# Performance work log

Hardware: AMD Instinct MI355X
Metric: run time of the kernel (lower is better)

Reference implementation:

```python
import jax, jax.numpy as jnp
import numpy as np

N = 50000      # nodes
E = 800000     # edges
NIN = 512      # input features
NHID = 128     # hidden
NCLS = 64      # classes


def setup_inputs() -> dict:
    key = jax.random.key(0)
    k0, k1, k2, k3 = jax.random.split(key, 4)
    x = jax.random.normal(k0, (N, NIN), dtype=jnp.float32)
    edge_index = jax.random.randint(k1, (2, E), 0, N, dtype=jnp.int64)
    # Glorot-style init for GCNConv linear weights (bias starts at zero in PyG)
    W1 = jax.random.normal(k2, (NIN, NHID), dtype=jnp.float32) * (1.0 / np.sqrt(NIN))
    W2 = jax.random.normal(k3, (NHID, NCLS), dtype=jnp.float32) * (1.0 / np.sqrt(NHID))
    b1 = jnp.zeros((NHID,), dtype=jnp.float32)
    b2 = jnp.zeros((NCLS,), dtype=jnp.float32)
    return {"x": x, "edge_index": edge_index, "W1": W1, "b1": b1, "W2": W2, "b2": b2}


def gcn_conv(x, W, b, src, dst, n):
    """PyG GCNConv: linear transform, then sym-normalized aggregation with self-loops."""
    xw = x @ W                                                  # [n, out]
    ones = jnp.ones(src.shape[0], dtype=xw.dtype)
    deg = jax.ops.segment_sum(ones, dst, num_segments=n) + 1.0  # +1 for self-loop
    dinv = jax.lax.rsqrt(deg)                                   # deg >= 1
    norm = dinv[src] * dinv[dst]                                # [E]
    agg = jax.ops.segment_sum(xw[src] * norm[:, None], dst, num_segments=n)
    agg = agg + (dinv * dinv)[:, None] * xw                     # self-loop messages
    return agg + b


def reference(x, edge_index, W1, b1, W2, b2):
    src, dst = edge_index[0], edge_index[1]
    n = x.shape[0]
    # eval mode: dropout is a no-op; bn is defined but unused in forward
    h = gcn_conv(x, W1, b1, src, dst, n)
    h = jax.nn.relu(h)
    o = gcn_conv(h, W2, b2, src, dst, n)
    return jax.nn.log_softmax(o, axis=1)
```

## Files before the change

### kernel.cpp

```cpp
#include <hip/hip_runtime.h>
#include <hip/hip_bf16.h>
#include <cstdint>
#include <cstddef>

#define NNODES 50000
#define NEDGES 800000
#define NIN    512
#define NHID   128
#define NCLS   64

#define SCAN_BLK 512
#define SCAN_NB ((NNODES + SCAN_BLK - 1) / SCAN_BLK)

typedef __attribute__((ext_vector_type(8))) short bf16x8;
typedef __attribute__((ext_vector_type(4))) float f32x4;

static __device__ __forceinline__ ushort f2bf(float f) {
    uint32_t u = __float_as_uint(f);
    uint32_t r = (u + 0x7fffu + ((u >> 16) & 1u)) >> 16;
    return (ushort)r;
}
static __device__ __forceinline__ float bf2f(ushort b) {
    return __uint_as_float(((uint32_t)b) << 16);
}

__global__ void clear_kernel(int4* __restrict__ p, int n4) {
    int i = blockIdx.x * blockDim.x + threadIdx.x;
    if (i < n4) p[i] = make_int4(0, 0, 0, 0);
}


__global__ void deg_kernel(const int* __restrict__ dst, int* __restrict__ deg) {
    int e = blockIdx.x * blockDim.x + threadIdx.x;
    if (e < NEDGES) atomicAdd(&deg[dst[e]], 1);
}

__global__ __launch_bounds__(SCAN_BLK) void scan1_kernel(const int* __restrict__ deg,
                                                         int* __restrict__ blkSum,
                                                         float* __restrict__ dinv) {
    int i = blockIdx.x * SCAN_BLK + threadIdx.x;
    int d = (i < NNODES) ? deg[i] : 0;
    if (i < NNODES) dinv[i] = rsqrtf((float)d + 1.0f);
    int v = d;
#pragma unroll
    for (int off = 32; off; off >>= 1) v += __shfl_xor(v, off, 64);
    __shared__ int ws[SCAN_BLK / 64];
    int w = threadIdx.x >> 6;
    if ((threadIdx.x & 63) == 0) ws[w] = v;
    __syncthreads();
    if (threadIdx.x == 0) {
        int s = 0;
#pragma unroll
        for (int k = 0; k < SCAN_BLK / 64; ++k) s += ws[k];
        blkSum[blockIdx.x] = s;
    }
}

__global__ void scan2_kernel(int* __restrict__ blkSum, int* __restrict__ rowptr) {
    __shared__ int sh[128];
    int t = threadIdx.x;
    int v = (t < SCAN_NB) ? blkSum[t] : 0;
    sh[t] = v;
    __syncthreads();
    for (int off = 1; off < 128; off <<= 1) {
        int o = (t >= off) ? sh[t - off] : 0;
        __syncthreads();
        sh[t] += o;
        __syncthreads();
    }
    if (t < SCAN_NB) blkSum[t] = sh[t] - v;
    if (t == 0) rowptr[NNODES] = NEDGES;
}

__global__ __launch_bounds__(SCAN_BLK) void scan3_kernel(const int* __restrict__ deg,
                                                         const int* __restrict__ blkOff,
                                                         int* __restrict__ rowptr) {
    int i = blockIdx.x * SCAN_BLK + threadIdx.x;
    int v = (i < NNODES) ? deg[i] : 0;
    int lane = threadIdx.x & 63;
    int w = threadIdx.x >> 6;
    int inc = v;
#pragma unroll
    for (int off = 1; off < 64; off <<= 1) {
        int o = __shfl_up(inc, off, 64);
        if (lane >= off) inc += o;
    }
    __shared__ int ws[SCAN_BLK / 64];
    if (lane == 63) ws[w] = inc;
    __syncthreads();
    int wpre = 0;
    for (int k = 0; k < w; ++k) wpre += ws[k];
    if (i < NNODES) rowptr[i] = inc - v + wpre + blkOff[blockIdx.x];
}

__global__ void scatter_kernel(const int* __restrict__ src, const int* __restrict__ dst,
                               const int* __restrict__ rowptr, int* __restrict__ cursor,
                               const float* __restrict__ dinv, int2* __restrict__ csr) {
    int e = blockIdx.x * blockDim.x + threadIdx.x;
    if (e >= NEDGES) return;
    int d = dst[e];
    int s = src[e];
    int pos = rowptr[d] + atomicAdd(&cursor[d], 1);
    csr[pos] = make_int2(s, __float_as_int(dinv[s]));
}

template <int NOUT, int KS, int CF>
__global__ void pack_kernel(const float* __restrict__ W, ushort* __restrict__ pack) {
    int t = blockIdx.x * blockDim.x + threadIdx.x;
    if (t >= KS * CF * 64 * 8) return;
    int j = t & 7;
    int lane = (t >> 3) & 63;
    int cf = (t >> 9) % CF;
    int ks = t / (CF * 512);
    int k = ks * 32 + (lane >> 4) * 8 + j;
    int c = cf * 16 + (lane & 15);
    pack[t] = f2bf(W[(size_t)k * NOUT + c]);
}

__global__ __launch_bounds__(256) void gemm1_kernel(const float* __restrict__ A,
                                                    const ushort* __restrict__ packB,
                                                    ushort* __restrict__ C) {
    __shared__ float lds[2][64 * 64];
    const int t = threadIdx.x;
    const int lane = t & 63;
    const int w = t >> 6;
    const int rowBase = blockIdx.x * 64;
    const int rl = lane & 15;
    const int kg = lane >> 4;

    const int Rloc = (w << 2) + (lane >> 4);
    const int csw = ((lane & 15) << 4) ^ ((Rloc & 7) << 4);
    const char* Abase = (const char*)A;

    const int xr = (rl & 7) << 4;

    f32x4 acc[8];
#pragma unroll
    for (int cf = 0; cf < 8; ++cf) acc[cf] = (f32x4)(0.f);

    auto stage = [&](int buf, int chunk) {
#pragma unroll
        for (int r = 0; r < 4; ++r) {
            int row = rowBase + r * 16 + Rloc;
            if (row > NNODES - 1) row = NNODES - 1;
            const char* src = Abase + (size_t)row * (NIN * 4) + chunk * 256 + csw;
            char* dst = (char*)&lds[buf][0] + r * 4096 + w * 1024 + lane * 16;
            __builtin_amdgcn_global_load_lds((const uint32_t*)src, (uint32_t*)dst, 16, 0, 0);
        }
    };

    stage(0, 0);
    int buf = 0;
#pragma unroll
    for (int tch = 0; tch < 8; ++tch) {
        __syncthreads();
        if (tch + 1 < 8) stage(buf ^ 1, tch + 1);
        const char* lrow = (const char*)&lds[buf][0] + (w * 16 + rl) * 256;
#pragma unroll
        for (int ks = 0; ks < 2; ++ks) {
            float4 x0 = *(const float4*)(lrow + ((ks * 128 + kg * 32) ^ xr));
            float4 x1 = *(const float4*)(lrow + ((ks * 128 + kg * 32 + 16) ^ xr));
            bf16x8 af;
            af[0] = (short)f2bf(x0.x); af[1] = (short)f2bf(x0.y);
            af[2] = (short)f2bf(x0.z); af[3] = (short)f2bf(x0.w);
            af[4] = (short)f2bf(x1.x); af[5] = (short)f2bf(x1.y);
            af[6] = (short)f2bf(x1.z); af[7] = (short)f2bf(x1.w);
            const ushort* bpp = packB + ((size_t)(tch * 2 + ks) * 8) * 512 + (size_t)lane * 8;
#pragma unroll
            for (int cf = 0; cf < 8; ++cf) {
                bf16x8 bfv = *(const bf16x8*)(bpp + cf * 512);
                acc[cf] = __builtin_amdgcn_mfma_f32_16x16x32_bf16(af, bfv, acc[cf], 0, 0, 0);
            }
        }
        buf ^= 1;
    }
    const int rowW = rowBase + w * 16;
#pragma unroll
    for (int cf = 0; cf < 8; ++cf)
#pragma unroll
        for (int j = 0; j < 4; ++j) {
            int rr = rowW + kg * 4 + j;
            if (rr < NNODES) C[(size_t)rr * NHID + cf * 16 + rl] = f2bf(acc[cf][j]);
        }
}

__global__ __launch_bounds__(256) void gemm2_kernel(const ushort* __restrict__ A,
                                                    const ushort* __restrict__ packB,
                                                    ushort* __restrict__ C) {
    int wid = (blockIdx.x * blockDim.x + threadIdx.x) >> 6;
    int lane = threadIdx.x & 63;
    int rowBase = wid * 16;
    if (rowBase >= NNODES) return;
    int rl = lane & 15;
    int kg = lane >> 4;
    const ushort* ap = A + (size_t)(rowBase + rl) * NHID + kg * 8;

    f32x4 acc[4];
#pragma unroll
    for (int cf = 0; cf < 4; ++cf) acc[cf] = (f32x4)(0.f);

#pragma unroll
    for (int ks = 0; ks < 4; ++ks) {
        bf16x8 af = *(const bf16x8*)(ap + ks * 32);
        const ushort* bp = packB + ((size_t)(ks * 4) * 64 + lane) * 8;
#pragma unroll
        for (int cf = 0; cf < 4; ++cf) {
            bf16x8 bf = *(const bf16x8*)(bp + (size_t)cf * 512);
            acc[cf] = __builtin_amdgcn_mfma_f32_16x16x32_bf16(af, bf, acc[cf], 0, 0, 0);
        }
    }
#pragma unroll
    for (int cf = 0; cf < 4; ++cf)
#pragma unroll
        for (int j = 0; j < 4; ++j)
            C[(size_t)(rowBase + kg * 4 + j) * NCLS + cf * 16 + rl] = f2bf(acc[cf][j]);
}

__global__ __launch_bounds__(256) void agg1_kernel(const ushort* __restrict__ xw,
                                                   const int* __restrict__ rowptr,
                                                   const int2* __restrict__ csr,
                                                   const float* __restrict__ dinv,
                                                   const float* __restrict__ b1,
                                                   ushort* __restrict__ h) {
    int wid = (blockIdx.x * blockDim.x + threadIdx.x) >> 6;
    int lane = threadIdx.x & 63;
    if (wid >= NNODES) return;
    int beg = rowptr[wid], end = rowptr[wid + 1];
    float a0 = 0.f, a1 = 0.f;
    int j = beg;
    for (; j + 8 <= end; j += 8) {
        int2 e[8];
#pragma unroll
        for (int q = 0; q < 8; ++q) e[q] = csr[j + q];
        uint v[8];
#pragma unroll
        for (int q = 0; q < 8; ++q) v[q] = *(const uint*)&xw[(size_t)e[q].x * NHID + lane * 2];
#pragma unroll
        for (int q = 0; q < 8; ++q) {
            float wq = __int_as_float(e[q].y);
            a0 += wq * __uint_as_float(v[q] << 16);
            a1 += wq * __uint_as_float(v[q] & 0xffff0000u);
        }
    }
    for (; j < end; ++j) {
        int2 e = csr[j];
        float w = __int_as_float(e.y);
        uint v = *(const uint*)&xw[(size_t)e.x * NHID + lane * 2];
        a0 += w * __uint_as_float(v << 16);
        a1 += w * __uint_as_float(v & 0xffff0000u);
    }
    float di = dinv[wid];
    float sl = di * di;
    uint xv = *(const uint*)&xw[(size_t)wid * NHID + lane * 2];
    float2 bv = *(const float2*)&b1[lane * 2];
    float r0 = di * a0 + sl * __uint_as_float(xv << 16) + bv.x;
    float r1 = di * a1 + sl * __uint_as_float(xv & 0xffff0000u) + bv.y;
    uint o = (uint)f2bf(fmaxf(r0, 0.f)) | ((uint)f2bf(fmaxf(r1, 0.f)) << 16);
    *(uint*)&h[(size_t)wid * NHID + lane * 2] = o;
}

__global__ __launch_bounds__(256) void agg2_kernel(const ushort* __restrict__ xw,
                                                   const int* __restrict__ rowptr,
                                                   const int2* __restrict__ csr,
                                                   const float* __restrict__ dinv,
                                                   const float* __restrict__ b2,
                                                   float* __restrict__ out) {
    int wid = (blockIdx.x * blockDim.x + threadIdx.x) >> 6;
    int lane = threadIdx.x & 63;
    if (wid >= NNODES) return;
    int beg = rowptr[wid], end = rowptr[wid + 1];
    float a = 0.f;
    int j = beg;
    for (; j + 8 <= end; j += 8) {
        int2 e[8];
#pragma unroll
        for (int q = 0; q < 8; ++q) e[q] = csr[j + q];
        float v[8];
#pragma unroll
        for (int q = 0; q < 8; ++q) v[q] = bf2f(xw[(size_t)e[q].x * NCLS + lane]);
#pragma unroll
        for (int q = 0; q < 8; ++q) a += __int_as_float(e[q].y) * v[q];
    }
    for (; j < end; ++j) {
        int2 e = csr[j];
        a += __int_as_float(e.y) * bf2f(xw[(size_t)e.x * NCLS + lane]);
    }
    float di = dinv[wid];
    float o = di * a + di * di * bf2f(xw[(size_t)wid * NCLS + lane]) + b2[lane];
    float m = o;
#pragma unroll
    for (int off = 32; off; off >>= 1) m = fmaxf(m, __shfl_xor(m, off, 64));
    float ex = __expf(o - m);
    float ssum = ex;
#pragma unroll
    for (int off = 32; off; off >>= 1) ssum += __shfl_xor(ssum, off, 64);
    out[(size_t)wid * NCLS + lane] = (o - m) - __logf(ssum);
}


extern "C" void kernel_launch(void* const* d_in, const int* in_sizes, int n_in,
                              void* d_out, int out_size, void* d_ws, size_t ws_size,
                              hipStream_t stream) {
    const float* x  = (const float*)d_in[0];
    const int*   ei = (const int*)d_in[1];
    const int*   src = ei;
    const int*   dst = ei + NEDGES;
    const float* W1 = (const float*)d_in[2];
    const float* b1 = (const float*)d_in[3];
    const float* W2 = (const float*)d_in[4];
    const float* b2 = (const float*)d_in[5];
    float* out = (float*)d_out;

    char* w = (char*)d_ws;
    auto alloc = [&](size_t bytes) {
        char* p = w;
        w += (bytes + 255) & ~(size_t)255;
        return p;
    };
    int*    deg    = (int*)alloc((size_t)2 * NNODES * 4);
    int*    cursor = deg + NNODES;
    int*    rowptr = (int*)alloc((NNODES + 1) * 4);
    int*    blkSum = (int*)alloc(SCAN_NB * 4);
    int2*   csr    = (int2*)alloc((size_t)NEDGES * 8);
    float*  dinv   = (float*)alloc(NNODES * 4);
    ushort* pack1  = (ushort*)alloc((size_t)16 * 8 * 64 * 8 * 2);
    ushort* pack2  = (ushort*)alloc((size_t)4 * 4 * 64 * 8 * 2);
    ushort* xw1    = (ushort*)alloc((size_t)NNODES * NHID * 2);
    ushort* h      = (ushort*)alloc((size_t)NNODES * NHID * 2);
    ushort* xw2    = (ushort*)alloc((size_t)NNODES * NCLS * 2);

    const int n4 = (2 * NNODES + 3) / 4;
    clear_kernel<<<(n4 + 255) / 256, 256, 0, stream>>>((int4*)deg, n4);

    deg_kernel<<<(NEDGES + 255) / 256, 256, 0, stream>>>(dst, deg);
    scan1_kernel<<<SCAN_NB, SCAN_BLK, 0, stream>>>(deg, blkSum, dinv);
    scan2_kernel<<<1, 128, 0, stream>>>(blkSum, rowptr);
    scan3_kernel<<<SCAN_NB, SCAN_BLK, 0, stream>>>(deg, blkSum, rowptr);
    scatter_kernel<<<(NEDGES + 255) / 256, 256, 0, stream>>>(src, dst, rowptr, cursor, dinv, csr);

    pack_kernel<NHID, 16, 8><<<(16 * 8 * 64 * 8 + 255) / 256, 256, 0, stream>>>(W1, pack1);
    pack_kernel<NCLS, 4, 4><<<(4 * 4 * 64 * 8 + 255) / 256, 256, 0, stream>>>(W2, pack2);

    gemm1_kernel<<<(NNODES + 63) / 64, 256, 0, stream>>>(x, pack1, xw1);
    agg1_kernel<<<(NNODES * 64 + 255) / 256, 256, 0, stream>>>(xw1, rowptr, csr, dinv, b1, h);

    gemm2_kernel<<<(NNODES / 16 + 3) / 4, 256, 0, stream>>>(h, pack2, xw2);
    agg2_kernel<<<(NNODES * 64 + 255) / 256, 256, 0, stream>>>(xw2, rowptr, csr, dinv, b2, out);
}
```

Before: 209.5 us.

## Split gemm1 K across waves with LDS reduction instead of LDS-staged row tiles

Restructures the first GEMM so each block handles 16 rows, with each of the 4 waves taking a 128-wide K slice. Each wave loads its x values directly from global memory into registers, and the partial MFMA accumulators are reduced through shared memory by wave 0. This removes the double-buffered global_load_lds staging and its per-chunk barriers, and puts all of x's loads in flight at once. The cost is more blocks, B fragments re-read by every block (four times less reuse per block), a reduction step, and wave 0 alone writing the output.

```diff
diff --git a/kernel.cpp b/kernel.cpp
--- a/kernel.cpp
+++ b/kernel.cpp
@@ -120,68 +120,62 @@
 __global__ __launch_bounds__(256) void gemm1_kernel(const float* __restrict__ A,
                                                     const ushort* __restrict__ packB,
                                                     ushort* __restrict__ C) {
-    __shared__ float lds[2][64 * 64];
+    __shared__ f32x4 red[3][8][64];
     const int t = threadIdx.x;
     const int lane = t & 63;
     const int w = t >> 6;
-    const int rowBase = blockIdx.x * 64;
+    const int rowBase = blockIdx.x * 16;
     const int rl = lane & 15;
     const int kg = lane >> 4;
-
-    const int Rloc = (w << 2) + (lane >> 4);
-    const int csw = ((lane & 15) << 4) ^ ((Rloc & 7) << 4);
-    const char* Abase = (const char*)A;
-
-    const int xr = (rl & 7) << 4;
+    const float* ap = A + (size_t)(rowBase + rl) * NIN + w * 128 + kg * 8;
+
+    float4 xv[8];
+#pragma unroll
+    for (int ks = 0; ks < 4; ++ks) {
+        xv[2 * ks]     = *(const float4*)(ap + ks * 32);
+        xv[2 * ks + 1] = *(const float4*)(ap + ks * 32 + 4);
+    }
 
     f32x4 acc[8];
 #pragma unroll
     for (int cf = 0; cf < 8; ++cf) acc[cf] = (f32x4)(0.f);
 
-    auto stage = [&](int buf, int chunk) {
-#pragma unroll
-        for (int r = 0; r < 4; ++r) {
-            int row = rowBase + r * 16 + Rloc;
-            if (row > NNODES - 1) row = NNODES - 1;
-            const char* src = Abase + (size_t)row * (NIN * 4) + chunk * 256 + csw;
-            char* dst = (char*)&lds[buf][0] + r * 4096 + w * 1024 + lane * 16;
-            __builtin_amdgcn_global_load_lds((const uint32_t*)src, (uint32_t*)dst, 16, 0, 0);
+#pragma unroll
+    for (int ks = 0; ks < 4; ++ks) {
+        float4 x0 = xv[2 * ks], x1 = xv[2 * ks + 1];
+        bf16x8 af;
+        af[0] = (short)f2bf(x0.x); af[1] = (short)f2bf(x0.y);
+        af[2] = (short)f2bf(x0.z); af[3] = (short)f2bf(x0.w);
+        af[4] = (short)f2bf(x1.x); af[5] = (short)f2bf(x1.y);
+        af[6] = (short)f2bf(x1.z); af[7] = (short)f2bf(x1.w);
+        const ushort* bp = packB + ((size_t)((w * 4 + ks) * 8) * 64 + lane) * 8;
+#pragma unroll
+        for (int cf = 0; cf < 8; ++cf) {
+            bf16x8 bfv = *(const bf16x8*)(bp + cf * 512);
+            acc[cf] = __builtin_amdgcn_mfma_f32_16x16x32_bf16(af, bfv, acc[cf], 0, 0, 0);
         }
-    };
-
-    stage(0, 0);
-    int buf = 0;
-#pragma unroll
-    for (int tch = 0; tch < 8; ++tch) {
-        __syncthreads();
-        if (tch + 1 < 8) stage(buf ^ 1, tch + 1);
-        const char* lrow = (const char*)&lds[buf][0] + (w * 16 + rl) * 256;
-#pragma unroll
-        for (int ks = 0; ks < 2; ++ks) {
-            float4 x0 = *(const float4*)(lrow + ((ks * 128 + kg * 32) ^ xr));
-            float4 x1 = *(const float4*)(lrow + ((ks * 128 + kg * 32 + 16) ^ xr));
-            bf16x8 af;
-            af[0] = (short)f2bf(x0.x); af[1] = (short)f2bf(x0.y);
-            af[2] = (short)f2bf(x0.z); af[3] = (short)f2bf(x0.w);
-            af[4] = (short)f2bf(x1.x); af[5] = (short)f2bf(x1.y);
-            af[6] = (short)f2bf(x1.z); af[7] = (short)f2bf(x1.w);
-            const ushort* bpp = packB + ((size_t)(tch * 2 + ks) * 8) * 512 + (size_t)lane * 8;
-#pragma unroll
-            for (int cf = 0; cf < 8; ++cf) {
-                bf16x8 bfv = *(const bf16x8*)(bpp + cf * 512);
-                acc[cf] = __builtin_amdgcn_mfma_f32_16x16x32_bf16(af, bfv, acc[cf], 0, 0, 0);
+    }
+
+    if (w) {
+#pragma unroll
+        for (int cf = 0; cf < 8; ++cf) red[w - 1][cf][lane] = acc[cf];
+    }
+    __syncthreads();
+    if (w == 0) {
+#pragma unroll
+        for (int cf = 0; cf < 8; ++cf)
+#pragma unroll
+            for (int q = 0; q < 3; ++q) {
+                f32x4 v = red[q][cf][lane];
+                acc[cf][0] += v[0]; acc[cf][1] += v[1];
+                acc[cf][2] += v[2]; acc[cf][3] += v[3];
             }
-        }
-        buf ^= 1;
-    }
-    const int rowW = rowBase + w * 16;
-#pragma unroll
-    for (int cf = 0; cf < 8; ++cf)
-#pragma unroll
-        for (int j = 0; j < 4; ++j) {
-            int rr = rowW + kg * 4 + j;
-            if (rr < NNODES) C[(size_t)rr * NHID + cf * 16 + rl] = f2bf(acc[cf][j]);
-        }
+#pragma unroll
+        for (int cf = 0; cf < 8; ++cf)
+#pragma unroll
+            for (int j = 0; j < 4; ++j)
+                C[(size_t)(rowBase + kg * 4 + j) * NHID + cf * 16 + rl] = f2bf(acc[cf][j]);
+    }
 }
 
 __global__ __launch_bounds__(256) void gemm2_kernel(const ushort* __restrict__ A,
@@ -341,7 +335,7 @@
     pack_kernel<NHID, 16, 8><<<(16 * 8 * 64 * 8 + 255) / 256, 256, 0, stream>>>(W1, pack1);
     pack_kernel<NCLS, 4, 4><<<(4 * 4 * 64 * 8 + 255) / 256, 256, 0, stream>>>(W2, pack2);
 
-    gemm1_kernel<<<(NNODES + 63) / 64, 256, 0, stream>>>(x, pack1, xw1);
+    gemm1_kernel<<<NNODES / 16, 256, 0, stream>>>(x, pack1, xw1);
     agg1_kernel<<<(NNODES * 64 + 255) / 256, 256, 0, stream>>>(xw1, rowptr, csr, dinv, b1, h);
 
     gemm2_kernel<<<(NNODES / 16 + 3) / 4, 256, 0, stream>>>(h, pack2, xw2);
```

Result: slower. 215.7 us (+3.0%).

## Keep W1 fragments in registers and stage A as bf16 in LDS for gemm1

Applied to the files above, without the earlier changes.

Restructures gemm1 so each wave owns two 16-column output slices across all 64 rows and holds its entire slice of packed W1 in registers, instead of re-reading B from global memory on every k-step. The A tile is now loaded into registers, converted to bf16 once and written to a swizzled bf16 LDS buffer, replacing the async fp32 global-to-LDS copy followed by per-wave conversion. This halves LDS footprint and removes repeated B loads and redundant conversions. The cost is high register pressure from 32 B fragments plus accumulators, and prefetch latency is now hidden through registers under explicit waitcnt and barriers.

```diff
diff --git a/kernel.cpp b/kernel.cpp
--- a/kernel.cpp
+++ b/kernel.cpp
@@ -22,6 +22,10 @@
 }
 static __device__ __forceinline__ float bf2f(ushort b) {
     return __uint_as_float(((uint32_t)b) << 16);
+}
+
+static __device__ __forceinline__ unsigned ldsAddr(const void* p) {
+    return (unsigned)(size_t)(__attribute__((address_space(3))) const void*)p;
 }
 
 __global__ void clear_kernel(int4* __restrict__ p, int n4) {
@@ -117,10 +121,10 @@
     pack[t] = f2bf(W[(size_t)k * NOUT + c]);
 }
 
-__global__ __launch_bounds__(256) void gemm1_kernel(const float* __restrict__ A,
-                                                    const ushort* __restrict__ packB,
-                                                    ushort* __restrict__ C) {
-    __shared__ float lds[2][64 * 64];
+__global__ __launch_bounds__(256, 2) void gemm1_kernel(const float* __restrict__ A,
+                                                       const ushort* __restrict__ packB,
+                                                       ushort* __restrict__ C) {
+    __shared__ ushort lds[2][64 * 64];
     const int t = threadIdx.x;
     const int lane = t & 63;
     const int w = t >> 6;
@@ -128,60 +132,106 @@
     const int rl = lane & 15;
     const int kg = lane >> 4;
 
-    const int Rloc = (w << 2) + (lane >> 4);
-    const int csw = ((lane & 15) << 4) ^ ((Rloc & 7) << 4);
-    const char* Abase = (const char*)A;
-
-    const int xr = (rl & 7) << 4;
-
-    f32x4 acc[8];
-#pragma unroll
-    for (int cf = 0; cf < 8; ++cf) acc[cf] = (f32x4)(0.f);
-
-    auto stage = [&](int buf, int chunk) {
-#pragma unroll
-        for (int r = 0; r < 4; ++r) {
-            int row = rowBase + r * 16 + Rloc;
-            if (row > NNODES - 1) row = NNODES - 1;
-            const char* src = Abase + (size_t)row * (NIN * 4) + chunk * 256 + csw;
-            char* dst = (char*)&lds[buf][0] + r * 4096 + w * 1024 + lane * 16;
-            __builtin_amdgcn_global_load_lds((const uint32_t*)src, (uint32_t*)dst, 16, 0, 0);
-        }
+    bf16x8 bw[16][2];
+    {
+        const ushort* bbase = packB + (size_t)lane * 8;
+#pragma unroll
+        for (int ks = 0; ks < 16; ++ks)
+#pragma unroll
+            for (int q = 0; q < 2; ++q)
+                bw[ks][q] = *(const bf16x8*)(bbase + ks * 4096 + (2 * w + q) * 512);
+    }
+
+    f32x4 acc[4][2];
+#pragma unroll
+    for (int rg = 0; rg < 4; ++rg)
+#pragma unroll
+        for (int q = 0; q < 2; ++q) acc[rg][q] = (f32x4)(0.f);
+
+    const int r0 = t >> 3,         c0 = t & 7;
+    const int r1 = (t + 256) >> 3, c1 = (t + 256) & 7;
+    int g0 = rowBase + r0; if (g0 >= NNODES) g0 = NNODES - 1;
+    int g1 = rowBase + r1; if (g1 >= NNODES) g1 = NNODES - 1;
+    const float* ga0 = A + (size_t)g0 * NIN + c0 * 8;
+    const float* ga1 = A + (size_t)g1 * NIN + c1 * 8;
+    ushort* wd0 = &lds[0][0] + r0 * 64 + ((c0 ^ (r0 & 7)) * 8);
+    ushort* wd1 = &lds[0][0] + r1 * 64 + ((c1 ^ (r1 & 7)) * 8);
+
+    auto cvt8 = [](float4 a, float4 b) {
+        bf16x8 v;
+        v[0] = (short)f2bf(a.x); v[1] = (short)f2bf(a.y);
+        v[2] = (short)f2bf(a.z); v[3] = (short)f2bf(a.w);
+        v[4] = (short)f2bf(b.x); v[5] = (short)f2bf(b.y);
+        v[6] = (short)f2bf(b.z); v[7] = (short)f2bf(b.w);
+        return v;
     };
 
-    stage(0, 0);
-    int buf = 0;
+    {
+        float4 p0 = *(const float4*)(ga0);
+        float4 p1 = *(const float4*)(ga0 + 4);
+        float4 p2 = *(const float4*)(ga1);
+        float4 p3 = *(const float4*)(ga1 + 4);
+        *(bf16x8*)wd0 = cvt8(p0, p1);
+        *(bf16x8*)wd1 = cvt8(p2, p3);
+    }
+    asm volatile("s_waitcnt lgkmcnt(0)" ::: "memory");
+    __builtin_amdgcn_s_barrier();
+
 #pragma unroll
     for (int tch = 0; tch < 8; ++tch) {
-        __syncthreads();
-        if (tch + 1 < 8) stage(buf ^ 1, tch + 1);
-        const char* lrow = (const char*)&lds[buf][0] + (w * 16 + rl) * 256;
+        const int cur = tch & 1;
+        float4 p0, p1, p2, p3;
+        if (tch < 7) {
+            p0 = *(const float4*)(ga0 + (tch + 1) * 64);
+            p1 = *(const float4*)(ga0 + (tch + 1) * 64 + 4);
+            p2 = *(const float4*)(ga1 + (tch + 1) * 64);
+            p3 = *(const float4*)(ga1 + (tch + 1) * 64 + 4);
+            __builtin_amdgcn_sched_barrier(0);
+        }
+        const unsigned lbase = ldsAddr(&lds[cur][0]);
 #pragma unroll
         for (int ks = 0; ks < 2; ++ks) {
-            float4 x0 = *(const float4*)(lrow + ((ks * 128 + kg * 32) ^ xr));
-            float4 x1 = *(const float4*)(lrow + ((ks * 128 + kg * 32 + 16) ^ xr));
-            bf16x8 af;
-            af[0] = (short)f2bf(x0.x); af[1] = (short)f2bf(x0.y);
-            af[2] = (short)f2bf(x0.z); af[3] = (short)f2bf(x0.w);
-            af[4] = (short)f2bf(x1.x); af[5] = (short)f2bf(x1.y);
-            af[6] = (short)f2bf(x1.z); af[7] = (short)f2bf(x1.w);
-            const ushort* bpp = packB + ((size_t)(tch * 2 + ks) * 8) * 512 + (size_t)lane * 8;
-#pragma unroll
-            for (int cf = 0; cf < 8; ++cf) {
-                bf16x8 bfv = *(const bf16x8*)(bpp + cf * 512);
-                acc[cf] = __builtin_amdgcn_mfma_f32_16x16x32_bf16(af, bfv, acc[cf], 0, 0, 0);
+            bf16x8 af0, af1, af2, af3;
+            const unsigned sw = (unsigned)(((ks * 4 + kg) ^ (rl & 7)) * 16);
+            const unsigned a0 = lbase + (unsigned)((0 * 16 + rl) * 128) + sw;
+            const unsigned a1 = lbase + (unsigned)((1 * 16 + rl) * 128) + sw;
+            const unsigned a2 = lbase + (unsigned)((2 * 16 + rl) * 128) + sw;
+            const unsigned a3 = lbase + (unsigned)((3 * 16 + rl) * 128) + sw;
+            asm volatile("ds_read_b128 %0, %1" : "=&v"(af0) : "v"(a0));
+            asm volatile("ds_read_b128 %0, %1" : "=&v"(af1) : "v"(a1));
+            asm volatile("ds_read_b128 %0, %1" : "=&v"(af2) : "v"(a2));
+            asm volatile("ds_read_b128 %0, %1" : "=&v"(af3) : "v"(a3));
+            asm volatile("s_waitcnt lgkmcnt(0)" ::: "memory");
+            __builtin_amdgcn_sched_barrier(0);
+            const int kq = tch * 2 + ks;
+            acc[0][0] = __builtin_amdgcn_mfma_f32_16x16x32_bf16(af0, bw[kq][0], acc[0][0], 0, 0, 0);
+            acc[0][1] = __builtin_amdgcn_mfma_f32_16x16x32_bf16(af0, bw[kq][1], acc[0][1], 0, 0, 0);
+            acc[1][0] = __builtin_amdgcn_mfma_f32_16x16x32_bf16(af1, bw[kq][0], acc[1][0], 0, 0, 0);
+            acc[1][1] = __builtin_amdgcn_mfma_f32_16x16x32_bf16(af1, bw[kq][1], acc[1][1], 0, 0, 0);
+            acc[2][0] = __builtin_amdgcn_mfma_f32_16x16x32_bf16(af2, bw[kq][0], acc[2][0], 0, 0, 0);
+            acc[2][1] = __builtin_amdgcn_mfma_f32_16x16x32_bf16(af2, bw[kq][1], acc[2][1], 0, 0, 0);
+            acc[3][0] = __builtin_amdgcn_mfma_f32_16x16x32_bf16(af3, bw[kq][0], acc[3][0], 0, 0, 0);
+            acc[3][1] = __builtin_amdgcn_mfma_f32_16x16x32_bf16(af3, bw[kq][1], acc[3][1], 0, 0, 0);
+        }
+        if (tch < 7) {
+            const int nxt = cur ^ 1;
+            *(bf16x8*)(wd0 + nxt * 4096) = cvt8(p0, p1);
+            *(bf16x8*)(wd1 + nxt * 4096) = cvt8(p2, p3);
+        }
+        asm volatile("s_waitcnt lgkmcnt(0)" ::: "memory");
+        __builtin_amdgcn_s_barrier();
+    }
+
+#pragma unroll
+    for (int rg = 0; rg < 4; ++rg)
+#pragma unroll
+        for (int q = 0; q < 2; ++q)
+#pragma unroll
+            for (int j = 0; j < 4; ++j) {
+                int rr = rowBase + rg * 16 + kg * 4 + j;
+                if (rr < NNODES)
+                    C[(size_t)rr * NHID + (2 * w + q) * 16 + rl] = f2bf(acc[rg][q][j]);
             }
-        }
-        buf ^= 1;
-    }
-    const int rowW = rowBase + w * 16;
-#pragma unroll
-    for (int cf = 0; cf < 8; ++cf)
-#pragma unroll
-        for (int j = 0; j < 4; ++j) {
-            int rr = rowW + kg * 4 + j;
-            if (rr < NNODES) C[(size_t)rr * NHID + cf * 16 + rl] = f2bf(acc[cf][j]);
-        }
 }
 
 __global__ __launch_bounds__(256) void gemm2_kernel(const ushort* __restrict__ A,
```

Measured after the change: 204.8 us. -2.2%, faster.
